# Optimization experiments

Measured on AMD Instinct MI355X. Metric: run time of the kernel, lower is better.

## Reference

```python
import jax, jax.numpy as jnp
import numpy as np

D_MODEL = 1024; D_STATE = 128; EXPAND = 2; HEADDIM = 64
D_INNER = EXPAND * D_MODEL; NHEADS = D_INNER // HEADDIM; PF = 2  # param_factor for complex
BATCH = 2; SEQ = 2048
DT_MIN = 0.001; DT_MAX = 0.1


def setup_inputs() -> dict:
    key = jax.random.key(0)
    k = jax.random.split(key, 10)
    u = jax.random.normal(k[0], (BATCH, SEQ, D_MODEL), jnp.float32)
    in_proj_w = jax.random.normal(k[1], (2 * D_INNER, D_MODEL), jnp.float32) * (D_MODEL ** -0.5)
    dt_projs_weight = jax.random.normal(k[2], (NHEADS, D_INNER), jnp.float32) * 0.02
    dt_projs_bias = (jax.random.uniform(k[3], (NHEADS,), jnp.float32)
                     * (np.log(DT_MAX) - np.log(DT_MIN)) + np.log(DT_MIN)).astype(jnp.float32)
    x_proj_w = jax.random.normal(k[4], (NHEADS * (1 + 2 * D_STATE * PF), D_INNER), jnp.float32) * (D_INNER ** -0.5)
    A = jnp.stack([-jax.random.uniform(k[5], (NHEADS, D_STATE), dtype=jnp.float32),
                   jax.random.normal(k[6], (NHEADS, D_STATE), jnp.float32) * 0.1], axis=-1)  # (H,N,2)
    D = jnp.ones((NHEADS,), jnp.float32)
    norm_B_w = jnp.ones((2 * D_STATE,), jnp.float32)
    norm_C_w = jnp.ones((2 * D_STATE,), jnp.float32)
    out_proj_w = jax.random.normal(k[7], (D_MODEL, D_INNER), jnp.float32) * (D_INNER ** -0.5)
    return {"u": u, "in_proj_w": in_proj_w, "dt_projs_weight": dt_projs_weight,
            "dt_projs_bias": dt_projs_bias, "x_proj_w": x_proj_w, "A": A, "D": D,
            "norm_B_w": norm_B_w, "norm_C_w": norm_C_w, "out_proj_w": out_proj_w}


def _rms_norm(x, w, eps=1e-6):
    return x * jax.lax.rsqrt(jnp.mean(x * x, axis=-1, keepdims=True) + eps) * w


def reference(u, in_proj_w, dt_projs_weight, dt_projs_bias, x_proj_w, A, D,
              norm_B_w, norm_C_w, out_proj_w):
    Bsz, L, _ = u.shape
    xz = u @ in_proj_w.T                        # (B,L,2*d_inner)
    x, z = jnp.split(xz, 2, axis=-1)
    x = jax.nn.silu(x)                          # (B,L,d_inner)
    dt = jax.nn.softplus(x @ dt_projs_weight.T + dt_projs_bias)  # (B,L,H)

    BCp = (x @ x_proj_w.T).reshape(Bsz, L, NHEADS, -1)
    BC = BCp[..., :2 * D_STATE * PF].reshape(Bsz, L, NHEADS, 2, D_STATE, PF)
    Bn = _rms_norm(BC[..., 0, :, :].reshape(Bsz, L, NHEADS, D_STATE * PF), norm_B_w)
    Cn = _rms_norm(BC[..., 1, :, :].reshape(Bsz, L, NHEADS, D_STATE * PF), norm_C_w)
    Bn = Bn.reshape(Bsz, L, NHEADS, D_STATE, PF)
    Cn = Cn.reshape(Bsz, L, NHEADS, D_STATE, PF)
    Bc = jax.lax.complex(Bn[..., 0], Bn[..., 1])  # (B,L,H,N) complex64
    Cc = jax.lax.complex(Cn[..., 0], Cn[..., 1])
    Ac = jax.lax.complex(A[..., 0], A[..., 1])    # (H,N) complex64

    xh = x.reshape(Bsz, L, NHEADS, HEADDIM)
    x_sum = xh.sum(axis=-1)                       # (B,L,H) -- kernel sums x_t over headdim
    zt = Ac[None, None] * (0.5 * dt)[..., None]   # (B,L,H,N) complex: A*dt/2
    den = 1.0 - zt
    abar = (1.0 + zt) / den                       # bilinear (Tustin) discretization
    u_in = Bc * ((dt * x_sum)[..., None] / den)   # Bbar * sum(x_t)

    def step(h, inp):
        a, b = inp
        h = a * h + b
        return h, h

    h0 = jnp.zeros((Bsz, NHEADS, D_STATE), jnp.complex64)
    _, hs = jax.lax.scan(step, h0, (jnp.swapaxes(abar, 0, 1), jnp.swapaxes(u_in, 0, 1)))
    hs = jnp.swapaxes(hs, 0, 1)                   # (B,L,H,N)
    y_red = jnp.real(Cc * hs).sum(axis=-1)        # (B,L,H), Re(C*h) reduced over state
    y = (xh * (y_red + D)[..., None]).reshape(Bsz, L, D_INNER)
    y = y * jax.nn.silu(z)
    return y @ out_proj_w.T
```

## Files before the change

### kernel.cpp

```cpp
#include <hip/hip_runtime.h>

#define BATCH   2
#define SEQ     2048
#define DMODEL  1024
#define DINNER  2048
#define NHEADS  32
#define HEADDIM 64
#define DSTATE  128
#define BLTOT   (BATCH * SEQ)
#define NCHUNK  32
#define CHUNK   64

#define OFF_UB   0ull
#define OFF_WXZ  8388608ull
#define OFF_WBC  16777216ull
#define OFF_WOUT 83886080ull
#define OFF_XB   88080384ull
#define OFF_YB   104857600ull
#define OFF_BC   121634816ull
#define OFF_SZ   255852544ull
#define OFF_DT   289406976ull
#define OFF_XS   289931264ull
#define OFF_YR   290455552ull
#define OFF_CA   291504128ull
#define OFF_CS   293601280ull
#define OFF_HI   295698432ull

typedef __attribute__((ext_vector_type(8))) short bf16x8;
typedef __attribute__((ext_vector_type(4))) float f32x4;

__device__ __forceinline__ float b2f(unsigned short u) {
    return __uint_as_float(((unsigned)u) << 16);
}
__device__ __forceinline__ unsigned short f2b(float f) {
    unsigned x = __float_as_uint(f);
    unsigned r = (x + 0x7fffu + ((x >> 16) & 1u)) >> 16;
    return (unsigned short)r;
}
__device__ __forceinline__ float silu_f(float v) {
    return v / (1.0f + __expf(-v));
}
__device__ __forceinline__ float softplus_f(float v) {
    return (v > 20.0f) ? v : log1pf(__expf(v));
}

__device__ __forceinline__ void gload_lds16(const void* g, void* l) {
    __builtin_amdgcn_global_load_lds(
        (const __attribute__((address_space(1))) unsigned int*)g,
        (__attribute__((address_space(3))) unsigned int*)l, 16, 0, 0);
}

__global__ __launch_bounds__(256) void f2b_kernel(
    const float* __restrict__ in, unsigned short* __restrict__ out) {
    int i = (blockIdx.x * 256 + threadIdx.x) * 4;
    float4 v = *(const float4*)&in[i];
    ushort4 o = {f2b(v.x), f2b(v.y), f2b(v.z), f2b(v.w)};
    *(ushort4*)&out[i] = o;
}

__global__ __launch_bounds__(256) void pack_xpw_kernel(
    const float* __restrict__ in, unsigned short* __restrict__ out) {
    int idx = blockIdx.x * 256 + threadIdx.x;
    int i = idx * 4;
    int c = i >> 11;
    int k = i & 2047;
    const float* src = in + ((size_t)(c >> 9) * 513 + (c & 511)) * 2048 + k;
    float4 v = *(const float4*)src;
    ushort4 o = {f2b(v.x), f2b(v.y), f2b(v.z), f2b(v.w)};
    *(ushort4*)&out[i] = o;
}

template <int K, int MODE>
__global__ __launch_bounds__(256) void gemm_mfma(
    const unsigned short* __restrict__ A, const unsigned short* __restrict__ B,
    void* __restrict__ C0, void* __restrict__ C1, int N) {
    __shared__ short ldsA[128 * 32];
    __shared__ short ldsB[128 * 32];
    int tid = threadIdx.x;
    int row0 = blockIdx.y * 128, col0 = blockIdx.x * 128;
    int lane = tid & 63, wave = tid >> 6;
    int wrow = (wave >> 1) * 64, wcol = (wave & 1) * 64;
    int m = lane & 15, quad = lane >> 4;

    f32x4 acc[4][4];
#pragma unroll
    for (int i = 0; i < 4; ++i)
#pragma unroll
        for (int j = 0; j < 4; ++j) acc[i][j] = (f32x4){0.f, 0.f, 0.f, 0.f};

    int r = tid >> 2, c8 = (tid & 3) * 8;
    const unsigned short* Ag = A + (size_t)(row0 + r) * K + c8;
    const unsigned short* Bg = B + (size_t)(col0 + r) * K + c8;
    short* la = ldsA + tid * 8;
    short* lb = ldsB + tid * 8;

    for (int k0 = 0; k0 < K; k0 += 32) {
        gload_lds16(Ag + k0, la);
        gload_lds16(Ag + (size_t)64 * K + k0, la + 2048);
        gload_lds16(Bg + k0, lb);
        gload_lds16(Bg + (size_t)64 * K + k0, lb + 2048);
        __syncthreads();
        bf16x8 af[4], bfr[4];
#pragma unroll
        for (int i = 0; i < 4; ++i)
            af[i] = *(const bf16x8*)&ldsA[(wrow + i * 16 + m) * 32 + quad * 8];
#pragma unroll
        for (int j = 0; j < 4; ++j)
            bfr[j] = *(const bf16x8*)&ldsB[(wcol + j * 16 + m) * 32 + quad * 8];
#pragma unroll
        for (int i = 0; i < 4; ++i)
#pragma unroll
            for (int j = 0; j < 4; ++j)
                acc[i][j] = __builtin_amdgcn_mfma_f32_16x16x32_bf16(
                    af[i], bfr[j], acc[i][j], 0, 0, 0);
        __syncthreads();
    }

#pragma unroll
    for (int i = 0; i < 4; ++i) {
#pragma unroll
        for (int reg = 0; reg < 4; ++reg) {
            int row = row0 + wrow + i * 16 + quad * 4 + reg;
#pragma unroll
            for (int j = 0; j < 4; ++j) {
                int col = col0 + wcol + j * 16 + m;
                float v = acc[i][j][reg];
                if (MODE == 0) {
                    ((float*)C0)[(size_t)row * N + col] = v;
                } else if (MODE == 1) {
                    float s = silu_f(v);
                    if (col < DINNER)
                        ((unsigned short*)C0)[(size_t)row * DINNER + col] = f2b(s);
                    else
                        ((float*)C1)[(size_t)row * DINNER + (col - DINNER)] = s;
                } else {
                    ((unsigned short*)C0)[(size_t)row * N + col] = f2b(v);
                }
            }
        }
    }
}

__global__ __launch_bounds__(256) void dt_xsum_kernel(
    const unsigned short* __restrict__ x, const float* __restrict__ dtw,
    const float* __restrict__ dtb, float* __restrict__ dt,
    float* __restrict__ xsum) {
    __shared__ float xs[DINNER];
    int bl = blockIdx.x;
    const unsigned short* xr = x + (size_t)bl * DINNER;
    {
        int i0 = threadIdx.x * 8;
        ushort4 a = *(const ushort4*)&xr[i0];
        ushort4 b = *(const ushort4*)&xr[i0 + 4];
        xs[i0 + 0] = b2f(a.x); xs[i0 + 1] = b2f(a.y);
        xs[i0 + 2] = b2f(a.z); xs[i0 + 3] = b2f(a.w);
        xs[i0 + 4] = b2f(b.x); xs[i0 + 5] = b2f(b.y);
        xs[i0 + 6] = b2f(b.z); xs[i0 + 7] = b2f(b.w);
    }
    __syncthreads();

    int h = threadIdx.x >> 3, s = threadIdx.x & 7;
    float xa = 0.0f;
#pragma unroll
    for (int j = s; j < HEADDIM; j += 8) xa += xs[h * HEADDIM + j];

    float acc = 0.0f;
    const float* w = dtw + h * DINNER;
    for (int i = s; i < DINNER; i += 8) acc += xs[i] * w[i];

#pragma unroll
    for (int off = 1; off < 8; off <<= 1) {
        acc += __shfl_xor(acc, off);
        xa  += __shfl_xor(xa, off);
    }
    if (s == 0) {
        dt[bl * NHEADS + h]   = softplus_f(acc + dtb[h]);
        xsum[bl * NHEADS + h] = xa;
    }
}

__global__ __launch_bounds__(256) void rmsnorm_kernel(
    unsigned short* __restrict__ bc, const float* __restrict__ wB,
    const float* __restrict__ wC) {
    int g = blockIdx.x * 4 + (threadIdx.x >> 6);
    int lane = threadIdx.x & 63;
    int cb = g & 1;
    unsigned short* p = bc + (size_t)g * 256 + lane * 4;
    ushort4 v = *(ushort4*)p;
    float f0 = b2f(v.x), f1 = b2f(v.y), f2 = b2f(v.z), f3 = b2f(v.w);
    float ss = f0 * f0 + f1 * f1 + f2 * f2 + f3 * f3;
#pragma unroll
    for (int off = 1; off < 64; off <<= 1) ss += __shfl_xor(ss, off);
    float scale = rsqrtf(ss * (1.0f / 256.0f) + 1e-6f);
    const float* w = (cb ? wC : wB) + lane * 4;
    float4 wv = *(const float4*)w;
    ushort4 o = {f2b(f0 * scale * wv.x), f2b(f1 * scale * wv.y),
                 f2b(f2 * scale * wv.z), f2b(f3 * scale * wv.w)};
    *(ushort4*)p = o;
}

__device__ __forceinline__ void step_coefs(
    float ar, float ai, float dtv, float xsv, unsigned bw,
    float& abr, float& abi, float& ur, float& ui) {
    float Br = b2f((unsigned short)(bw & 0xffff));
    float Bi = b2f((unsigned short)(bw >> 16));
    float hd = 0.5f * dtv;
    float ztr = ar * hd, zti = ai * hd;
    float denr = 1.0f - ztr;
    float s2 = 1.0f / (denr * denr + zti * zti);
    float invr = denr * s2, invi = zti * s2;
    float opr = 1.0f + ztr;
    abr = opr * invr - zti * invi;
    abi = opr * invi + zti * invr;
    float coef = dtv * xsv;
    float cr = coef * invr, ci = coef * invi;
    ur = Br * cr - Bi * ci;
    ui = Br * ci + Bi * cr;
}

__global__ __launch_bounds__(128) void scan_pass1(
    const unsigned short* __restrict__ bc, const float* __restrict__ dt,
    const float* __restrict__ xsum, const float* __restrict__ A,
    float2* __restrict__ cA, float2* __restrict__ cS) {
    int blk = blockIdx.x;
    int bh = blk >> 5, c = blk & (NCHUNK - 1);
    int b = bh >> 5, h = bh & 31;
    int n = threadIdx.x;
    float ar = A[(h * DSTATE + n) * 2 + 0];
    float ai = A[(h * DSTATE + n) * 2 + 1];
    int l0 = c * CHUNK;
    const unsigned short* base = bc + ((size_t)(b * SEQ + l0)) * 16384 + h * 512;
    const float* dtp = dt + (b * SEQ + l0) * NHEADS + h;
    const float* xsp = xsum + (b * SEQ + l0) * NHEADS + h;

    float pr = 1.f, pi = 0.f, sr = 0.f, si = 0.f;
    for (int l = 0; l < CHUNK; ++l) {
        unsigned bw = *(const unsigned*)&base[(size_t)l * 16384 + n * 2];
        float dtv = dtp[l * NHEADS], xsv = xsp[l * NHEADS];
        float abr, abi, ur, ui;
        step_coefs(ar, ai, dtv, xsv, bw, abr, abi, ur, ui);
        float nsr = abr * sr - abi * si + ur;
        float nsi = abr * si + abi * sr + ui;
        sr = nsr; si = nsi;
        float npr = abr * pr - abi * pi;
        float npi = abr * pi + abi * pr;
        pr = npr; pi = npi;
    }
    size_t idx = ((size_t)bh * NCHUNK + c) * DSTATE + n;
    cA[idx] = {pr, pi};
    cS[idx] = {sr, si};
}

__global__ __launch_bounds__(128) void scan_fixup(
    const float2* __restrict__ cA, const float2* __restrict__ cS,
    float2* __restrict__ hin) {
    int bh = blockIdx.x;
    int n = threadIdx.x;
    float hr = 0.f, hi = 0.f;
    for (int c = 0; c < NCHUNK; ++c) {
        size_t idx = ((size_t)bh * NCHUNK + c) * DSTATE + n;
        hin[idx] = {hr, hi};
        float2 a = cA[idx];
        float2 s = cS[idx];
        float nhr = a.x * hr - a.y * hi + s.x;
        float nhi = a.x * hi + a.y * hr + s.y;
        hr = nhr; hi = nhi;
    }
}

__global__ __launch_bounds__(128) void scan_pass2(
    const unsigned short* __restrict__ bc, const float* __restrict__ dt,
    const float* __restrict__ xsum, const float* __restrict__ A,
    const float2* __restrict__ hin, float* __restrict__ yredp) {
    int blk = blockIdx.x;
    int bh = blk >> 5, c = blk & (NCHUNK - 1);
    int b = bh >> 5, h = bh & 31;
    int n = threadIdx.x;
    float ar = A[(h * DSTATE + n) * 2 + 0];
    float ai = A[(h * DSTATE + n) * 2 + 1];
    int l0 = c * CHUNK;
    const unsigned short* base = bc + ((size_t)(b * SEQ + l0)) * 16384 + h * 512;
    const float* dtp = dt + (b * SEQ + l0) * NHEADS + h;
    const float* xsp = xsum + (b * SEQ + l0) * NHEADS + h;
    int wv = n >> 6, lane = n & 63;
    float* yp = yredp + ((size_t)(b * SEQ + l0) * NHEADS + h) * 2 + wv;

    float2 h0 = hin[((size_t)bh * NCHUNK + c) * DSTATE + n];
    float hr = h0.x, hi = h0.y;
    for (int l = 0; l < CHUNK; ++l) {
        unsigned bw = *(const unsigned*)&base[(size_t)l * 16384 + n * 2];
        unsigned cw = *(const unsigned*)&base[(size_t)l * 16384 + 256 + n * 2];
        float dtv = dtp[l * NHEADS], xsv = xsp[l * NHEADS];
        float abr, abi, ur, ui;
        step_coefs(ar, ai, dtv, xsv, bw, abr, abi, ur, ui);
        float nhr = abr * hr - abi * hi + ur;
        float nhi = abr * hi + abi * hr + ui;
        hr = nhr; hi = nhi;
        float Cr = b2f((unsigned short)(cw & 0xffff));
        float Ci = b2f((unsigned short)(cw >> 16));
        float y = Cr * hr - Ci * hi;
#pragma unroll
        for (int off = 1; off < 64; off <<= 1) y += __shfl_xor(y, off);
        if (lane == 0) yp[(size_t)l * (NHEADS * 2)] = y;
    }
}

__global__ __launch_bounds__(256) void yfuse_kernel(
    const unsigned short* __restrict__ x, const float* __restrict__ sz,
    const float* __restrict__ yredp, const float* __restrict__ Dv,
    unsigned short* __restrict__ y) {
    int i = (blockIdx.x * 256 + threadIdx.x) * 4;
    int r = i >> 11;
    int k = i & (DINNER - 1);
    int h = k >> 6;
    float yr = yredp[(r * NHEADS + h) * 2 + 0] +
               yredp[(r * NHEADS + h) * 2 + 1] + Dv[h];
    ushort4 xv = *(const ushort4*)&x[i];
    float4 zv = *(const float4*)&sz[i];
    ushort4 o = {f2b(b2f(xv.x) * yr * zv.x), f2b(b2f(xv.y) * yr * zv.y),
                 f2b(b2f(xv.z) * yr * zv.z), f2b(b2f(xv.w) * yr * zv.w)};
    *(ushort4*)&y[i] = o;
}

extern "C" void kernel_launch(void* const* d_in, const int* in_sizes, int n_in,
                              void* d_out, int out_size, void* d_ws, size_t ws_size,
                              hipStream_t stream) {
    const float* u   = (const float*)d_in[0];
    const float* ipw = (const float*)d_in[1];
    const float* dtw = (const float*)d_in[2];
    const float* dtb = (const float*)d_in[3];
    const float* xpw = (const float*)d_in[4];
    const float* A   = (const float*)d_in[5];
    const float* Dv  = (const float*)d_in[6];
    const float* wB  = (const float*)d_in[7];
    const float* wC  = (const float*)d_in[8];
    const float* opw = (const float*)d_in[9];
    float* out = (float*)d_out;
    char* ws = (char*)d_ws;

    unsigned short* u_b   = (unsigned short*)(ws + OFF_UB);
    unsigned short* w_xz  = (unsigned short*)(ws + OFF_WXZ);
    unsigned short* w_bc  = (unsigned short*)(ws + OFF_WBC);
    unsigned short* w_out = (unsigned short*)(ws + OFF_WOUT);
    unsigned short* x_b   = (unsigned short*)(ws + OFF_XB);
    unsigned short* y_b   = (unsigned short*)(ws + OFF_YB);
    unsigned short* bc    = (unsigned short*)(ws + OFF_BC);
    float* sz    = (float*)(ws + OFF_SZ);
    float* dt    = (float*)(ws + OFF_DT);
    float* xsum  = (float*)(ws + OFF_XS);
    float* yredp = (float*)(ws + OFF_YR);
    float2* cA   = (float2*)(ws + OFF_CA);
    float2* cS   = (float2*)(ws + OFF_CS);
    float2* hin  = (float2*)(ws + OFF_HI);

    f2b_kernel<<<4096, 256, 0, stream>>>(u, u_b);
    f2b_kernel<<<4096, 256, 0, stream>>>(ipw, w_xz);
    f2b_kernel<<<2048, 256, 0, stream>>>(opw, w_out);
    pack_xpw_kernel<<<32768, 256, 0, stream>>>(xpw, w_bc);

    gemm_mfma<1024, 1><<<dim3(32, 32), 256, 0, stream>>>(u_b, w_xz, x_b, sz, 4096);
    dt_xsum_kernel<<<BLTOT, 256, 0, stream>>>(x_b, dtw, dtb, dt, xsum);
    gemm_mfma<2048, 2><<<dim3(128, 32), 256, 0, stream>>>(x_b, w_bc, bc, nullptr, 16384);
    rmsnorm_kernel<<<BLTOT * NHEADS * 2 / 4, 256, 0, stream>>>(bc, wB, wC);

    scan_pass1<<<BATCH * NHEADS * NCHUNK, 128, 0, stream>>>(bc, dt, xsum, A, cA, cS);
    scan_fixup<<<BATCH * NHEADS, 128, 0, stream>>>(cA, cS, hin);
    scan_pass2<<<BATCH * NHEADS * NCHUNK, 128, 0, stream>>>(bc, dt, xsum, A, hin, yredp);

    yfuse_kernel<<<BLTOT * DINNER / 4 / 256, 256, 0, stream>>>(x_b, sz, yredp, Dv, y_b);
    gemm_mfma<2048, 0><<<dim3(8, 32), 256, 0, stream>>>(y_b, w_out, out, nullptr, 1024);
}
```

Measured before the change: 879.6 us.

## Fuse conversions, xsum into GEMM epilogue, RMSNorm into scans, bf16 gate

Merges the four weight and input conversion launches into one kernel. The per-head x sum moves into the in_proj GEMM epilogue, and dt becomes a tiled LDS dot-product kernel. The separate RMSNorm pass over B/C is removed and the normalisation is recomputed inside both scan passes, which now use one 64-lane wave handling two states per thread. The silu(z) gate is stored as bf16 instead of fp32. The intent is fewer launches and less memory traffic, at the cost of redundant normalisation work in the scans and lower precision for the gate.

```diff
diff --git a/kernel.cpp b/kernel.cpp
--- a/kernel.cpp
+++ b/kernel.cpp
@@ -19,12 +19,12 @@
 #define OFF_YB   104857600ull
 #define OFF_BC   121634816ull
 #define OFF_SZ   255852544ull
-#define OFF_DT   289406976ull
-#define OFF_XS   289931264ull
-#define OFF_YR   290455552ull
-#define OFF_CA   291504128ull
-#define OFF_CS   293601280ull
-#define OFF_HI   295698432ull
+#define OFF_DT   272629760ull
+#define OFF_XS   273154048ull
+#define OFF_YR   273678336ull
+#define OFF_CA   274202624ull
+#define OFF_CS   276299776ull
+#define OFF_HI   278396928ull
 
 typedef __attribute__((ext_vector_type(8))) short bf16x8;
 typedef __attribute__((ext_vector_type(4))) float f32x4;
@@ -50,30 +50,37 @@
         (__attribute__((address_space(3))) unsigned int*)l, 16, 0, 0);
 }
 
-__global__ __launch_bounds__(256) void f2b_kernel(
-    const float* __restrict__ in, unsigned short* __restrict__ out) {
-    int i = (blockIdx.x * 256 + threadIdx.x) * 4;
-    float4 v = *(const float4*)&in[i];
+__global__ __launch_bounds__(256) void conv_all_kernel(
+    const float* __restrict__ u, const float* __restrict__ ipw,
+    const float* __restrict__ opw, const float* __restrict__ xpw,
+    unsigned short* __restrict__ u_b, unsigned short* __restrict__ w_xz,
+    unsigned short* __restrict__ w_out, unsigned short* __restrict__ w_bc) {
+    long idx = (long)blockIdx.x * 256 + threadIdx.x;
+    if (idx >= 2621440L) {
+        long e = (idx - 2621440L) * 4;
+        long c = e >> 11, k = e & 2047;
+        const float* s = xpw + ((c >> 9) * 513 + (c & 511)) * 2048 + k;
+        float4 v = *(const float4*)s;
+        ushort4 o = {f2b(v.x), f2b(v.y), f2b(v.z), f2b(v.w)};
+        *(ushort4*)&w_bc[e] = o;
+        return;
+    }
+    const float* src;
+    unsigned short* dst;
+    long i;
+    if (idx < 1048576L)      { src = u;   dst = u_b;   i = idx; }
+    else if (idx < 2097152L) { src = ipw; dst = w_xz;  i = idx - 1048576L; }
+    else                     { src = opw; dst = w_out; i = idx - 2097152L; }
+    float4 v = *(const float4*)&src[i * 4];
     ushort4 o = {f2b(v.x), f2b(v.y), f2b(v.z), f2b(v.w)};
-    *(ushort4*)&out[i] = o;
-}
-
-__global__ __launch_bounds__(256) void pack_xpw_kernel(
-    const float* __restrict__ in, unsigned short* __restrict__ out) {
-    int idx = blockIdx.x * 256 + threadIdx.x;
-    int i = idx * 4;
-    int c = i >> 11;
-    int k = i & 2047;
-    const float* src = in + ((size_t)(c >> 9) * 513 + (c & 511)) * 2048 + k;
-    float4 v = *(const float4*)src;
-    ushort4 o = {f2b(v.x), f2b(v.y), f2b(v.z), f2b(v.w)};
-    *(ushort4*)&out[i] = o;
+    *(ushort4*)&dst[i * 4] = o;
 }
 
 template <int K, int MODE>
 __global__ __launch_bounds__(256) void gemm_mfma(
     const unsigned short* __restrict__ A, const unsigned short* __restrict__ B,
-    void* __restrict__ C0, void* __restrict__ C1, int N) {
+    void* __restrict__ C0, void* __restrict__ C1, float* __restrict__ C2,
+    int N) {
     __shared__ short ldsA[128 * 32];
     __shared__ short ldsB[128 * 32];
     int tid = threadIdx.x;
@@ -116,94 +123,117 @@
         __syncthreads();
     }
 
-#pragma unroll
-    for (int i = 0; i < 4; ++i) {
-#pragma unroll
-        for (int reg = 0; reg < 4; ++reg) {
-            int row = row0 + wrow + i * 16 + quad * 4 + reg;
-#pragma unroll
-            for (int j = 0; j < 4; ++j) {
-                int col = col0 + wcol + j * 16 + m;
-                float v = acc[i][j][reg];
-                if (MODE == 0) {
-                    ((float*)C0)[(size_t)row * N + col] = v;
-                } else if (MODE == 1) {
-                    float s = silu_f(v);
-                    if (col < DINNER)
+    if (MODE == 1) {
+        bool isx = (col0 < DINNER);
+        if (isx) {
+            int head = (col0 + wcol) >> 6;
+            float ssum[4][4];
+#pragma unroll
+            for (int i = 0; i < 4; ++i)
+#pragma unroll
+                for (int reg = 0; reg < 4; ++reg) ssum[i][reg] = 0.f;
+#pragma unroll
+            for (int i = 0; i < 4; ++i)
+#pragma unroll
+                for (int reg = 0; reg < 4; ++reg) {
+                    int row = row0 + wrow + i * 16 + quad * 4 + reg;
+#pragma unroll
+                    for (int j = 0; j < 4; ++j) {
+                        int col = col0 + wcol + j * 16 + m;
+                        float s = silu_f(acc[i][j][reg]);
                         ((unsigned short*)C0)[(size_t)row * DINNER + col] = f2b(s);
+                        ssum[i][reg] += s;
+                    }
+                }
+#pragma unroll
+            for (int i = 0; i < 4; ++i)
+#pragma unroll
+                for (int reg = 0; reg < 4; ++reg) {
+                    float s = ssum[i][reg];
+                    s += __shfl_xor(s, 1);
+                    s += __shfl_xor(s, 2);
+                    s += __shfl_xor(s, 4);
+                    s += __shfl_xor(s, 8);
+                    if (m == 0) {
+                        int row = row0 + wrow + i * 16 + quad * 4 + reg;
+                        C2[(size_t)row * NHEADS + head] = s;
+                    }
+                }
+        } else {
+#pragma unroll
+            for (int i = 0; i < 4; ++i)
+#pragma unroll
+                for (int reg = 0; reg < 4; ++reg) {
+                    int row = row0 + wrow + i * 16 + quad * 4 + reg;
+#pragma unroll
+                    for (int j = 0; j < 4; ++j) {
+                        int col = col0 + wcol + j * 16 + m - DINNER;
+                        float s = silu_f(acc[i][j][reg]);
+                        ((unsigned short*)C1)[(size_t)row * DINNER + col] = f2b(s);
+                    }
+                }
+        }
+    } else {
+#pragma unroll
+        for (int i = 0; i < 4; ++i)
+#pragma unroll
+            for (int reg = 0; reg < 4; ++reg) {
+                int row = row0 + wrow + i * 16 + quad * 4 + reg;
+#pragma unroll
+                for (int j = 0; j < 4; ++j) {
+                    int col = col0 + wcol + j * 16 + m;
+                    float v = acc[i][j][reg];
+                    if (MODE == 0)
+                        ((float*)C0)[(size_t)row * N + col] = v;
                     else
-                        ((float*)C1)[(size_t)row * DINNER + (col - DINNER)] = s;
-                } else {
-                    ((unsigned short*)C0)[(size_t)row * N + col] = f2b(v);
+                        ((unsigned short*)C0)[(size_t)row * N + col] = f2b(v);
                 }
             }
+    }
+}
+
+__global__ __launch_bounds__(256) void dt_kernel(
+    const unsigned short* __restrict__ x, const float* __restrict__ dtw,
+    const float* __restrict__ dtb, float* __restrict__ dt) {
+    __shared__ float xs[16][132];
+    __shared__ float ws[32][132];
+    int r0 = blockIdx.x * 16;
+    int t = threadIdx.x;
+    int lrow = t >> 4, lc8 = (t & 15) * 8;
+    int lh = t >> 3, lc16 = (t & 7) * 16;
+    int row = t >> 4, h0 = t & 15;
+    float acc0 = 0.f, acc1 = 0.f;
+
+    for (int kc = 0; kc < DINNER; kc += 128) {
+        ushort4 a = *(const ushort4*)&x[(size_t)(r0 + lrow) * DINNER + kc + lc8];
+        ushort4 b = *(const ushort4*)&x[(size_t)(r0 + lrow) * DINNER + kc + lc8 + 4];
+        xs[lrow][lc8 + 0] = b2f(a.x); xs[lrow][lc8 + 1] = b2f(a.y);
+        xs[lrow][lc8 + 2] = b2f(a.z); xs[lrow][lc8 + 3] = b2f(a.w);
+        xs[lrow][lc8 + 4] = b2f(b.x); xs[lrow][lc8 + 5] = b2f(b.y);
+        xs[lrow][lc8 + 6] = b2f(b.z); xs[lrow][lc8 + 7] = b2f(b.w);
+#pragma unroll
+        for (int q = 0; q < 4; ++q) {
+            float4 w = *(const float4*)&dtw[(size_t)lh * DINNER + kc + lc16 + q * 4];
+            *(float4*)&ws[lh][lc16 + q * 4] = w;
         }
-    }
-}
-
-__global__ __launch_bounds__(256) void dt_xsum_kernel(
-    const unsigned short* __restrict__ x, const float* __restrict__ dtw,
-    const float* __restrict__ dtb, float* __restrict__ dt,
-    float* __restrict__ xsum) {
-    __shared__ float xs[DINNER];
-    int bl = blockIdx.x;
-    const unsigned short* xr = x + (size_t)bl * DINNER;
-    {
-        int i0 = threadIdx.x * 8;
-        ushort4 a = *(const ushort4*)&xr[i0];
-        ushort4 b = *(const ushort4*)&xr[i0 + 4];
-        xs[i0 + 0] = b2f(a.x); xs[i0 + 1] = b2f(a.y);
-        xs[i0 + 2] = b2f(a.z); xs[i0 + 3] = b2f(a.w);
-        xs[i0 + 4] = b2f(b.x); xs[i0 + 5] = b2f(b.y);
-        xs[i0 + 6] = b2f(b.z); xs[i0 + 7] = b2f(b.w);
-    }
-    __syncthreads();
-
-    int h = threadIdx.x >> 3, s = threadIdx.x & 7;
-    float xa = 0.0f;
-#pragma unroll
-    for (int j = s; j < HEADDIM; j += 8) xa += xs[h * HEADDIM + j];
-
-    float acc = 0.0f;
-    const float* w = dtw + h * DINNER;
-    for (int i = s; i < DINNER; i += 8) acc += xs[i] * w[i];
-
-#pragma unroll
-    for (int off = 1; off < 8; off <<= 1) {
-        acc += __shfl_xor(acc, off);
-        xa  += __shfl_xor(xa, off);
-    }
-    if (s == 0) {
-        dt[bl * NHEADS + h]   = softplus_f(acc + dtb[h]);
-        xsum[bl * NHEADS + h] = xa;
-    }
-}
-
-__global__ __launch_bounds__(256) void rmsnorm_kernel(
-    unsigned short* __restrict__ bc, const float* __restrict__ wB,
-    const float* __restrict__ wC) {
-    int g = blockIdx.x * 4 + (threadIdx.x >> 6);
-    int lane = threadIdx.x & 63;
-    int cb = g & 1;
-    unsigned short* p = bc + (size_t)g * 256 + lane * 4;
-    ushort4 v = *(ushort4*)p;
-    float f0 = b2f(v.x), f1 = b2f(v.y), f2 = b2f(v.z), f3 = b2f(v.w);
-    float ss = f0 * f0 + f1 * f1 + f2 * f2 + f3 * f3;
-#pragma unroll
-    for (int off = 1; off < 64; off <<= 1) ss += __shfl_xor(ss, off);
-    float scale = rsqrtf(ss * (1.0f / 256.0f) + 1e-6f);
-    const float* w = (cb ? wC : wB) + lane * 4;
-    float4 wv = *(const float4*)w;
-    ushort4 o = {f2b(f0 * scale * wv.x), f2b(f1 * scale * wv.y),
-                 f2b(f2 * scale * wv.z), f2b(f3 * scale * wv.w)};
-    *(ushort4*)p = o;
-}
-
-__device__ __forceinline__ void step_coefs(
-    float ar, float ai, float dtv, float xsv, unsigned bw,
+        __syncthreads();
+#pragma unroll
+        for (int k = 0; k < 128; k += 4) {
+            float4 xv = *(const float4*)&xs[row][k];
+            float4 w0 = *(const float4*)&ws[h0][k];
+            float4 w1 = *(const float4*)&ws[h0 + 16][k];
+            acc0 += xv.x * w0.x + xv.y * w0.y + xv.z * w0.z + xv.w * w0.w;
+            acc1 += xv.x * w1.x + xv.y * w1.y + xv.z * w1.z + xv.w * w1.w;
+        }
+        __syncthreads();
+    }
+    dt[(size_t)(r0 + row) * NHEADS + h0]      = softplus_f(acc0 + dtb[h0]);
+    dt[(size_t)(r0 + row) * NHEADS + h0 + 16] = softplus_f(acc1 + dtb[h0 + 16]);
+}
+
+__device__ __forceinline__ void coefs(
+    float ar, float ai, float dtv, float xsv, float Br, float Bi,
     float& abr, float& abi, float& ur, float& ui) {
-    float Br = b2f((unsigned short)(bw & 0xffff));
-    float Bi = b2f((unsigned short)(bw >> 16));
     float hd = 0.5f * dtv;
     float ztr = ar * hd, zti = ai * hd;
     float denr = 1.0f - ztr;
@@ -218,37 +248,56 @@
     ui = Br * ci + Bi * cr;
 }
 
-__global__ __launch_bounds__(128) void scan_pass1(
+__global__ __launch_bounds__(64) void scan_pass1(
     const unsigned short* __restrict__ bc, const float* __restrict__ dt,
     const float* __restrict__ xsum, const float* __restrict__ A,
-    float2* __restrict__ cA, float2* __restrict__ cS) {
+    const float* __restrict__ wB, float2* __restrict__ cA,
+    float2* __restrict__ cS) {
     int blk = blockIdx.x;
     int bh = blk >> 5, c = blk & (NCHUNK - 1);
     int b = bh >> 5, h = bh & 31;
-    int n = threadIdx.x;
-    float ar = A[(h * DSTATE + n) * 2 + 0];
-    float ai = A[(h * DSTATE + n) * 2 + 1];
+    int t = threadIdx.x;
+    float4 av = *(const float4*)&A[(h * DSTATE + 2 * t) * 2];
+    float4 wv = *(const float4*)&wB[4 * t];
     int l0 = c * CHUNK;
     const unsigned short* base = bc + ((size_t)(b * SEQ + l0)) * 16384 + h * 512;
     const float* dtp = dt + (b * SEQ + l0) * NHEADS + h;
     const float* xsp = xsum + (b * SEQ + l0) * NHEADS + h;
 
-    float pr = 1.f, pi = 0.f, sr = 0.f, si = 0.f;
+    float pr0 = 1.f, pi0 = 0.f, sr0 = 0.f, si0 = 0.f;
+    float pr1 = 1.f, pi1 = 0.f, sr1 = 0.f, si1 = 0.f;
     for (int l = 0; l < CHUNK; ++l) {
-        unsigned bw = *(const unsigned*)&base[(size_t)l * 16384 + n * 2];
+        uint2 bw = *(const uint2*)&base[(size_t)l * 16384 + 4 * t];
+        float Br0 = b2f((unsigned short)(bw.x & 0xffff));
+        float Bi0 = b2f((unsigned short)(bw.x >> 16));
+        float Br1 = b2f((unsigned short)(bw.y & 0xffff));
+        float Bi1 = b2f((unsigned short)(bw.y >> 16));
+        float ss = Br0 * Br0 + Bi0 * Bi0 + Br1 * Br1 + Bi1 * Bi1;
+#pragma unroll
+        for (int off = 1; off < 64; off <<= 1) ss += __shfl_xor(ss, off);
+        float scale = rsqrtf(ss * (1.0f / 256.0f) + 1e-6f);
+        Br0 *= scale * wv.x; Bi0 *= scale * wv.y;
+        Br1 *= scale * wv.z; Bi1 *= scale * wv.w;
         float dtv = dtp[l * NHEADS], xsv = xsp[l * NHEADS];
         float abr, abi, ur, ui;
-        step_coefs(ar, ai, dtv, xsv, bw, abr, abi, ur, ui);
-        float nsr = abr * sr - abi * si + ur;
-        float nsi = abr * si + abi * sr + ui;
-        sr = nsr; si = nsi;
-        float npr = abr * pr - abi * pi;
-        float npi = abr * pi + abi * pr;
-        pr = npr; pi = npi;
-    }
-    size_t idx = ((size_t)bh * NCHUNK + c) * DSTATE + n;
-    cA[idx] = {pr, pi};
-    cS[idx] = {sr, si};
+        coefs(av.x, av.y, dtv, xsv, Br0, Bi0, abr, abi, ur, ui);
+        float ns = abr * sr0 - abi * si0 + ur;
+        float nsi = abr * si0 + abi * sr0 + ui;
+        sr0 = ns; si0 = nsi;
+        float np = abr * pr0 - abi * pi0;
+        float npi = abr * pi0 + abi * pr0;
+        pr0 = np; pi0 = npi;
+        coefs(av.z, av.w, dtv, xsv, Br1, Bi1, abr, abi, ur, ui);
+        ns = abr * sr1 - abi * si1 + ur;
+        nsi = abr * si1 + abi * sr1 + ui;
+        sr1 = ns; si1 = nsi;
+        np = abr * pr1 - abi * pi1;
+        npi = abr * pi1 + abi * pr1;
+        pr1 = np; pi1 = npi;
+    }
+    size_t idx = ((size_t)bh * NCHUNK + c) * DSTATE + 2 * t;
+    *(float4*)&cA[idx] = (float4){pr0, pi0, pr1, pi1};
+    *(float4*)&cS[idx] = (float4){sr0, si0, sr1, si1};
 }
 
 __global__ __launch_bounds__(128) void scan_fixup(
@@ -268,57 +317,83 @@
     }
 }
 
-__global__ __launch_bounds__(128) void scan_pass2(
+__global__ __launch_bounds__(64) void scan_pass2(
     const unsigned short* __restrict__ bc, const float* __restrict__ dt,
     const float* __restrict__ xsum, const float* __restrict__ A,
+    const float* __restrict__ wB, const float* __restrict__ wC,
     const float2* __restrict__ hin, float* __restrict__ yredp) {
     int blk = blockIdx.x;
     int bh = blk >> 5, c = blk & (NCHUNK - 1);
     int b = bh >> 5, h = bh & 31;
-    int n = threadIdx.x;
-    float ar = A[(h * DSTATE + n) * 2 + 0];
-    float ai = A[(h * DSTATE + n) * 2 + 1];
+    int t = threadIdx.x;
+    float4 av = *(const float4*)&A[(h * DSTATE + 2 * t) * 2];
+    float4 wbv = *(const float4*)&wB[4 * t];
+    float4 wcv = *(const float4*)&wC[4 * t];
     int l0 = c * CHUNK;
     const unsigned short* base = bc + ((size_t)(b * SEQ + l0)) * 16384 + h * 512;
     const float* dtp = dt + (b * SEQ + l0) * NHEADS + h;
     const float* xsp = xsum + (b * SEQ + l0) * NHEADS + h;
-    int wv = n >> 6, lane = n & 63;
-    float* yp = yredp + ((size_t)(b * SEQ + l0) * NHEADS + h) * 2 + wv;
-
-    float2 h0 = hin[((size_t)bh * NCHUNK + c) * DSTATE + n];
-    float hr = h0.x, hi = h0.y;
+    float* yp = yredp + (size_t)(b * SEQ + l0) * NHEADS + h;
+
+    float4 h0v = *(const float4*)&hin[((size_t)bh * NCHUNK + c) * DSTATE + 2 * t];
+    float hr0 = h0v.x, hi0 = h0v.y, hr1 = h0v.z, hi1 = h0v.w;
+
     for (int l = 0; l < CHUNK; ++l) {
-        unsigned bw = *(const unsigned*)&base[(size_t)l * 16384 + n * 2];
-        unsigned cw = *(const unsigned*)&base[(size_t)l * 16384 + 256 + n * 2];
+        uint2 bw = *(const uint2*)&base[(size_t)l * 16384 + 4 * t];
+        uint2 cw = *(const uint2*)&base[(size_t)l * 16384 + 256 + 4 * t];
+        float Br0 = b2f((unsigned short)(bw.x & 0xffff));
+        float Bi0 = b2f((unsigned short)(bw.x >> 16));
+        float Br1 = b2f((unsigned short)(bw.y & 0xffff));
+        float Bi1 = b2f((unsigned short)(bw.y >> 16));
+        float Cr0 = b2f((unsigned short)(cw.x & 0xffff));
+        float Ci0 = b2f((unsigned short)(cw.x >> 16));
+        float Cr1 = b2f((unsigned short)(cw.y & 0xffff));
+        float Ci1 = b2f((unsigned short)(cw.y >> 16));
+        float ssB = Br0 * Br0 + Bi0 * Bi0 + Br1 * Br1 + Bi1 * Bi1;
+        float ssC = Cr0 * Cr0 + Ci0 * Ci0 + Cr1 * Cr1 + Ci1 * Ci1;
+#pragma unroll
+        for (int off = 1; off < 64; off <<= 1) {
+            ssB += __shfl_xor(ssB, off);
+            ssC += __shfl_xor(ssC, off);
+        }
+        float sB = rsqrtf(ssB * (1.0f / 256.0f) + 1e-6f);
+        float sC = rsqrtf(ssC * (1.0f / 256.0f) + 1e-6f);
+        Br0 *= sB * wbv.x; Bi0 *= sB * wbv.y;
+        Br1 *= sB * wbv.z; Bi1 *= sB * wbv.w;
+        Cr0 *= sC * wcv.x; Ci0 *= sC * wcv.y;
+        Cr1 *= sC * wcv.z; Ci1 *= sC * wcv.w;
         float dtv = dtp[l * NHEADS], xsv = xsp[l * NHEADS];
         float abr, abi, ur, ui;
-        step_coefs(ar, ai, dtv, xsv, bw, abr, abi, ur, ui);
-        float nhr = abr * hr - abi * hi + ur;
-        float nhi = abr * hi + abi * hr + ui;
-        hr = nhr; hi = nhi;
-        float Cr = b2f((unsigned short)(cw & 0xffff));
-        float Ci = b2f((unsigned short)(cw >> 16));
-        float y = Cr * hr - Ci * hi;
+        coefs(av.x, av.y, dtv, xsv, Br0, Bi0, abr, abi, ur, ui);
+        float nhr = abr * hr0 - abi * hi0 + ur;
+        float nhi = abr * hi0 + abi * hr0 + ui;
+        hr0 = nhr; hi0 = nhi;
+        coefs(av.z, av.w, dtv, xsv, Br1, Bi1, abr, abi, ur, ui);
+        nhr = abr * hr1 - abi * hi1 + ur;
+        nhi = abr * hi1 + abi * hr1 + ui;
+        hr1 = nhr; hi1 = nhi;
+        float y = Cr0 * hr0 - Ci0 * hi0 + Cr1 * hr1 - Ci1 * hi1;
 #pragma unroll
         for (int off = 1; off < 64; off <<= 1) y += __shfl_xor(y, off);
-        if (lane == 0) yp[(size_t)l * (NHEADS * 2)] = y;
+        if (t == 0) yp[(size_t)l * NHEADS] = y;
     }
 }
 
 __global__ __launch_bounds__(256) void yfuse_kernel(
-    const unsigned short* __restrict__ x, const float* __restrict__ sz,
+    const unsigned short* __restrict__ x, const unsigned short* __restrict__ sz,
     const float* __restrict__ yredp, const float* __restrict__ Dv,
     unsigned short* __restrict__ y) {
     int i = (blockIdx.x * 256 + threadIdx.x) * 4;
     int r = i >> 11;
     int k = i & (DINNER - 1);
     int h = k >> 6;
-    float yr = yredp[(r * NHEADS + h) * 2 + 0] +
-               yredp[(r * NHEADS + h) * 2 + 1] + Dv[h];
+    float yr = yredp[(size_t)r * NHEADS + h] + Dv[h];
     ushort4 xv = *(const ushort4*)&x[i];
-    float4 zv = *(const float4*)&sz[i];
-    ushort4 o = {f2b(b2f(xv.x) * yr * zv.x), f2b(b2f(xv.y) * yr * zv.y),
-                 f2b(b2f(xv.z) * yr * zv.z), f2b(b2f(xv.w) * yr * zv.w)};
+    ushort4 zv = *(const ushort4*)&sz[i];
+    ushort4 o = {f2b(b2f(xv.x) * yr * b2f(zv.x)),
+                 f2b(b2f(xv.y) * yr * b2f(zv.y)),
+                 f2b(b2f(xv.z) * yr * b2f(zv.z)),
+                 f2b(b2f(xv.w) * yr * b2f(zv.w))};
     *(ushort4*)&y[i] = o;
 }
 
@@ -345,7 +420,7 @@
     unsigned short* x_b   = (unsigned short*)(ws + OFF_XB);
     unsigned short* y_b   = (unsigned short*)(ws + OFF_YB);
     unsigned short* bc    = (unsigned short*)(ws + OFF_BC);
-    float* sz    = (float*)(ws + OFF_SZ);
+    unsigned short* sz    = (unsigned short*)(ws + OFF_SZ);
     float* dt    = (float*)(ws + OFF_DT);
     float* xsum  = (float*)(ws + OFF_XS);
     float* yredp = (float*)(ws + OFF_YR);
@@ -353,20 +428,23 @@
     float2* cS   = (float2*)(ws + OFF_CS);
     float2* hin  = (float2*)(ws + OFF_HI);
 
-    f2b_kernel<<<4096, 256, 0, stream>>>(u, u_b);
-    f2b_kernel<<<4096, 256, 0, stream>>>(ipw, w_xz);
-    f2b_kernel<<<2048, 256, 0, stream>>>(opw, w_out);
-    pack_xpw_kernel<<<32768, 256, 0, stream>>>(xpw, w_bc);
-
-    gemm_mfma<1024, 1><<<dim3(32, 32), 256, 0, stream>>>(u_b, w_xz, x_b, sz, 4096);
-    dt_xsum_kernel<<<BLTOT, 256, 0, stream>>>(x_b, dtw, dtb, dt, xsum);
-    gemm_mfma<2048, 2><<<dim3(128, 32), 256, 0, stream>>>(x_b, w_bc, bc, nullptr, 16384);
-    rmsnorm_kernel<<<BLTOT * NHEADS * 2 / 4, 256, 0, stream>>>(bc, wB, wC);
-
-    scan_pass1<<<BATCH * NHEADS * NCHUNK, 128, 0, stream>>>(bc, dt, xsum, A, cA, cS);
+    conv_all_kernel<<<43008, 256, 0, stream>>>(u, ipw, opw, xpw,
+                                               u_b, w_xz, w_out, w_bc);
+
+    gemm_mfma<1024, 1><<<dim3(32, 32), 256, 0, stream>>>(
+        u_b, w_xz, x_b, sz, xsum, 4096);
+    dt_kernel<<<BLTOT / 16, 256, 0, stream>>>(x_b, dtw, dtb, dt);
+    gemm_mfma<2048, 2><<<dim3(128, 32), 256, 0, stream>>>(
+        x_b, w_bc, bc, nullptr, nullptr, 16384);
+
+    scan_pass1<<<BATCH * NHEADS * NCHUNK, 64, 0, stream>>>(
+        bc, dt, xsum, A, wB, cA, cS);
     scan_fixup<<<BATCH * NHEADS, 128, 0, stream>>>(cA, cS, hin);
-    scan_pass2<<<BATCH * NHEADS * NCHUNK, 128, 0, stream>>>(bc, dt, xsum, A, hin, yredp);
-
-    yfuse_kernel<<<BLTOT * DINNER / 4 / 256, 256, 0, stream>>>(x_b, sz, yredp, Dv, y_b);
-    gemm_mfma<2048, 0><<<dim3(8, 32), 256, 0, stream>>>(y_b, w_out, out, nullptr, 1024);
-}
+    scan_pass2<<<BATCH * NHEADS * NCHUNK, 64, 0, stream>>>(
+        bc, dt, xsum, A, wB, wC, hin, yredp);
+
+    yfuse_kernel<<<BLTOT * DINNER / 4 / 256, 256, 0, stream>>>(
+        x_b, sz, yredp, Dv, y_b);
+    gemm_mfma<2048, 0><<<dim3(8, 32), 256, 0, stream>>>(
+        y_b, w_out, out, nullptr, nullptr, 1024);
+}
```

New measurement: 837.5 us. -4.8%, faster.
